# Kernel optimization log

Hardware: AMD Instinct MI355X
Metric: run time of the kernel (lower is better)

## Reference

```python
import jax, jax.numpy as jnp
import numpy as np

NUM_HEADS = 16
THETA = 10000.0


def _rope(x, pos):
    # x: (B, H, S, d_k), pos: (B, S) int
    d_k = x.shape[-1]
    freqs = 1.0 / (THETA ** (jnp.arange(0, d_k, 2, dtype=jnp.float32) / d_k))  # (d_k/2,)
    angles = pos[..., None].astype(jnp.float32) * freqs  # (B, S, d_k/2)
    cos = jnp.cos(angles)[:, None, :, :]  # (B, 1, S, d_k/2) broadcast over heads
    sin = jnp.sin(angles)[:, None, :, :]
    x1 = x[..., 0::2]
    x2 = x[..., 1::2]
    out1 = x1 * cos - x2 * sin
    out2 = x1 * sin + x2 * cos
    # interleave back: (..., d_k/2, 2) -> (..., d_k)
    return jnp.stack((out1, out2), axis=-1).reshape(x.shape)


def setup_inputs() -> dict:
    key = jax.random.key(0)
    ks = jax.random.split(key, 6)
    B, S, D = 4, 2048, 1024
    x = jax.random.normal(ks[0], (B, S, D), dtype=jnp.float32)
    token_positions = jnp.sort(jax.random.randint(ks[1], (B, S), 0, S), axis=-1).astype(jnp.int32)
    Wq = jax.random.normal(ks[2], (D, D), dtype=jnp.float32) * (D ** -0.5)
    Wk = jax.random.normal(ks[3], (D, D), dtype=jnp.float32) * (D ** -0.5)
    Wv = jax.random.normal(ks[4], (D, D), dtype=jnp.float32) * (D ** -0.5)
    Wo = jax.random.normal(ks[5], (D, D), dtype=jnp.float32) * (D ** -0.5)
    return {"x": x, "token_positions": token_positions, "Wq": Wq, "Wk": Wk, "Wv": Wv, "Wo": Wo}


def reference(x, token_positions, Wq, Wk, Wv, Wo):
    B, S, D = x.shape
    H = NUM_HEADS
    d_k = D // H
    # projections: y = x @ W.T  (Linear stores weight as (d_out, d_in))
    q = jnp.einsum('bsd,od->bso', x, Wq).reshape(B, S, H, d_k).transpose(0, 2, 1, 3)
    k = jnp.einsum('bsd,od->bso', x, Wk).reshape(B, S, H, d_k).transpose(0, 2, 1, 3)
    v = jnp.einsum('bsd,od->bso', x, Wv).reshape(B, S, H, d_k).transpose(0, 2, 1, 3)
    q = _rope(q, token_positions)
    k = _rope(k, token_positions)
    scores = jnp.einsum('bhqd,bhkd->bhqk', q, k) / jnp.sqrt(jnp.float32(d_k))
    causal = jnp.tril(jnp.ones((S, S), dtype=bool))
    scores = jnp.where(causal, scores, -jnp.inf)
    attn = jax.nn.softmax(scores, axis=-1)
    attn = jnp.nan_to_num(attn, nan=0.0)
    out = jnp.einsum('bhqk,bhkd->bhqd', attn, v)
    out = out.transpose(0, 2, 1, 3).reshape(B, S, D)
    return jnp.einsum('bso,do->bsd', out, Wo)
```

## Files before the change

### kernel.cpp

```cpp
#include <hip/hip_runtime.h>
#include <stdint.h>

#define SEQ 2048
#define NH  16
#define DK  64
#define DM  1024
#define C2SM 0.18033688011112042f

typedef __bf16 bf16x8 __attribute__((ext_vector_type(8)));
typedef float  f32x4  __attribute__((ext_vector_type(4)));
typedef float  f32x16 __attribute__((ext_vector_type(16)));
typedef int    iv2    __attribute__((ext_vector_type(2)));
typedef void __attribute__((address_space(3))) lds_void;
typedef const void __attribute__((address_space(1))) glb_void;

__device__ __forceinline__ unsigned short f2b(float f) {
  unsigned int u = __float_as_uint(f);
  u += 0x7fffu + ((u >> 16) & 1u);
  return (unsigned short)(u >> 16);
}
__device__ __forceinline__ float b2f(unsigned short h) {
  return __uint_as_float(((unsigned int)h) << 16);
}
__device__ __forceinline__ void gload_lds16(const void* g, void* lds) {
  __builtin_amdgcn_global_load_lds((glb_void*)(uintptr_t)g,
                                   (lds_void*)(unsigned int)(uintptr_t)lds,
                                   16, 0, 0);
}
__device__ __forceinline__ unsigned int cvtpk(float lo, float hi) {
  unsigned int r;
  asm("v_cvt_pk_bf16_f32 %0, %1, %2" : "=v"(r) : "v"(lo), "v"(hi));
  return r;
}
__device__ __forceinline__ iv2 pl32swap(int a, int b) {
  return __builtin_amdgcn_permlane32_swap(a, b, false, false);
}

__global__ __launch_bounds__(256) void k_cvt(const float* __restrict__ src,
                                             unsigned short* __restrict__ dst, int n4) {
  int i = blockIdx.x * 256 + threadIdx.x;
  if (i >= n4) return;
  float4 v = ((const float4*)src)[i];
  uint2 o;
  o.x = (unsigned int)f2b(v.x) | ((unsigned int)f2b(v.y) << 16);
  o.y = (unsigned int)f2b(v.z) | ((unsigned int)f2b(v.w) << 16);
  ((uint2*)dst)[i] = o;
}

__global__ __launch_bounds__(256) void k_cvtw(const float* __restrict__ w0,
                                              const float* __restrict__ w1,
                                              const float* __restrict__ w2,
                                              const float* __restrict__ w3,
                                              unsigned short* __restrict__ dst) {
  int i = blockIdx.x * 256 + threadIdx.x;
  const float* s = (i < 524288) ? ((i < 262144) ? w0 : w1)
                                : ((i < 786432) ? w2 : w3);
  float4 v = ((const float4*)s)[i & 262143];
  uint2 o;
  o.x = (unsigned int)f2b(v.x) | ((unsigned int)f2b(v.y) << 16);
  o.y = (unsigned int)f2b(v.z) | ((unsigned int)f2b(v.w) << 16);
  ((uint2*)dst)[i] = o;
}

__global__ __launch_bounds__(256) void k_tab(float2* __restrict__ tab) {
  int i = blockIdx.x * 256 + threadIdx.x;
  int p = i >> 5, f = i & 31;
  float freq = powf(10000.0f, -(float)(2 * f) / (float)DK);
  float ang = (float)p * freq;
  tab[i] = make_float2(cosf(ang), sinf(ang));
}

template <int MODE>
__global__ __launch_bounds__(256) void k_gemm(const unsigned short* __restrict__ A,
                                              const unsigned short* __restrict__ B,
                                              void* __restrict__ C, void* __restrict__ C2,
                                              const int* __restrict__ pos,
                                              const float2* __restrict__ tab,
                                              int M, int N, int K) {
  __shared__ __align__(16) unsigned short As[3][4096];
  __shared__ __align__(16) unsigned short Bs[3][4096];
  const int tid = threadIdx.x;
  const int wid = tid >> 6, lane = tid & 63;
  const int lr = lane & 15, lk = lane >> 4;
  const int wr = wid >> 1, wc = wid & 1;
  const int m0 = blockIdx.x * 128, n0 = blockIdx.y * 128;
  const int r0 = tid >> 2;
  const int csw = (((tid & 3) ^ ((r0 >> 1) & 3)) << 3);
  const int ss = ((lk ^ ((lr >> 1) & 3)) << 3);
  f32x4 acc[4][4] = {};

#define GSTAGE(bi, k0)                                                       \
  do {                                                                       \
    gload_lds16(A + (size_t)(m0 + r0) * K + (k0) + csw, &As[bi][wid * 512]); \
    gload_lds16(A + (size_t)(m0 + 64 + r0) * K + (k0) + csw,                 \
                &As[bi][2048 + wid * 512]);                                  \
    gload_lds16(B + (size_t)(n0 + r0) * K + (k0) + csw, &Bs[bi][wid * 512]); \
    gload_lds16(B + (size_t)(n0 + 64 + r0) * K + (k0) + csw,                 \
                &Bs[bi][2048 + wid * 512]);                                  \
  } while (0)

  const int nt = K >> 5;
  GSTAGE(0, 0);
  if (nt > 1) {
    GSTAGE(1, 32);
    asm volatile("s_waitcnt vmcnt(4)" ::: "memory");
  } else {
    asm volatile("s_waitcnt vmcnt(0)" ::: "memory");
  }
  __builtin_amdgcn_s_barrier();
  int c0 = 0, c1 = 1, c2 = 2;
  for (int t = 0; t < nt; ++t) {
    if (t + 2 < nt) GSTAGE(c2, (t + 2) * 32);
    bf16x8 af[4], bfv[4];
#pragma unroll
    for (int i = 0; i < 4; ++i)
      af[i] = *(const bf16x8*)&As[c0][(wr * 64 + i * 16 + lr) * 32 + ss];
#pragma unroll
    for (int j = 0; j < 4; ++j)
      bfv[j] = *(const bf16x8*)&Bs[c0][(wc * 64 + j * 16 + lr) * 32 + ss];
    __builtin_amdgcn_s_setprio(1);
#pragma unroll
    for (int i = 0; i < 4; ++i)
#pragma unroll
      for (int j = 0; j < 4; ++j)
        acc[i][j] = __builtin_amdgcn_mfma_f32_16x16x32_bf16(af[i], bfv[j], acc[i][j], 0, 0, 0);
    __builtin_amdgcn_s_setprio(0);
    if (t + 1 < nt) {
      if (t + 2 < nt)
        asm volatile("s_waitcnt vmcnt(4)" ::: "memory");
      else
        asm volatile("s_waitcnt vmcnt(0)" ::: "memory");
      __builtin_amdgcn_s_barrier();
    }
    int tmp = c0; c0 = c1; c1 = c2; c2 = tmp;
  }
#undef GSTAGE

  if (MODE == 1) {
#pragma unroll
    for (int i = 0; i < 4; ++i) {
      const int rbase = m0 + wr * 64 + i * 16 + lk * 4;
#pragma unroll
      for (int j = 0; j < 4; ++j) {
        const int col = n0 + wc * 64 + j * 16 + lr;
#pragma unroll
        for (int r = 0; r < 4; ++r)
          ((float*)C)[(size_t)(rbase + r) * N + col] = acc[i][j][r];
      }
    }
  } else {
    const int tt = n0 >> 10;
    if (tt == 2) {
#pragma unroll
      for (int i = 0; i < 4; ++i) {
        const int rbase = m0 + wr * 64 + i * 16 + lk * 4;
        const int bb = rbase >> 11;
        const int s0 = rbase & (SEQ - 1);
#pragma unroll
        for (int j = 0; j < 4; ++j) {
          const int col = n0 + wc * 64 + j * 16 + lr;
          const int h = (col >> 6) & 15, d = col & 63;
          uint2 pv;
          pv.x = cvtpk(acc[i][j][0], acc[i][j][1]);
          pv.y = cvtpk(acc[i][j][2], acc[i][j][3]);
          *(uint2*)&((unsigned short*)C2)[(((size_t)bb * NH + h) * DK + d) * SEQ + s0] = pv;
        }
      }
    } else {
#pragma unroll
      for (int i = 0; i < 4; ++i) {
        const int rbase = m0 + wr * 64 + i * 16 + lk * 4;
        const int bb = rbase >> 11;
        int prr[4];
#pragma unroll
        for (int r = 0; r < 4; ++r)
          prr[r] = pos[bb * SEQ + ((rbase + r) & (SEQ - 1))];
#pragma unroll
        for (int j = 0; j < 4; ++j) {
          const int col = n0 + wc * 64 + j * 16 + lr;
          const int h = (col >> 6) & 15, d = col & 63;
          const int f = d >> 1;
#pragma unroll
          for (int r = 0; r < 4; ++r) {
            float v = acc[i][j][r];
            float pv = __shfl_xor(v, 1);
            float2 cs = tab[(size_t)prr[r] * 32 + f];
            float o = (d & 1) ? __builtin_fmaf(pv, cs.y, v * cs.x)
                              : __builtin_fmaf(-pv, cs.y, v * cs.x);
            const int s = (rbase + r) & (SEQ - 1);
            ((unsigned short*)C)[(size_t)tt * 8388608 +
                                 ((((size_t)bb * NH + h) * SEQ) + s) * DK + d] = f2b(o);
          }
        }
      }
    }
  }
}

__global__ __launch_bounds__(128) void k_attn(const unsigned short* __restrict__ Q,
                                              const unsigned short* __restrict__ K,
                                              const unsigned short* __restrict__ VT,
                                              unsigned short* __restrict__ O) {
  __shared__ __align__(16) unsigned short Ks[2][64 * 64];
  __shared__ __align__(16) unsigned short Vs[2][64 * 64];
  const int tid = threadIdx.x, wid = tid >> 6, lane = tid & 63;
  const int l31 = lane & 31, hi = lane >> 5;
  const int n = blockIdx.x;
  const int bh = n & 63;
  const int qt = 31 - (n >> 6);
  const unsigned short* Qp = Q + (size_t)bh * SEQ * DK;
  const unsigned short* Kp = K + (size_t)bh * SEQ * DK;
  const unsigned short* Vp = VT + (size_t)bh * DK * SEQ;
  const int b = bh >> 4, h = bh & (NH - 1);

#define STAGE(bi, kb)                                                          \
  do {                                                                         \
    _Pragma("unroll") for (int i = 0; i < 4; ++i) {                            \
      const int c = i * 128 + tid;                                             \
      const int row = c >> 3, sl = ((c & 7) ^ (row & 7)) << 3;                 \
      gload_lds16(Kp + (size_t)((kb) + row) * DK + sl,                         \
                  &Ks[bi][(i * 128 + wid * 64) * 8]);                          \
      gload_lds16(Vp + (size_t)row * SEQ + (kb) + sl,                          \
                  &Vs[bi][(i * 128 + wid * 64) * 8]);                          \
    }                                                                          \
  } while (0)

  const int qw = qt * 64 + wid * 32;
  const int qrow = qw + l31;
  bf16x8 qf[4];
#pragma unroll
  for (int ks = 0; ks < 4; ++ks)
    qf[ks] = *(const bf16x8*)&Qp[(size_t)qrow * DK + ks * 16 + hi * 8];
  f32x16 oacc[2] = {};
  float m_ = -1e30f, l_ = 0.f;
  const int ntiles = qt + 1;
  STAGE(0, 0);
  for (int kt = 0; kt < ntiles; ++kt) {
    const int cur = kt & 1;
    const int kb = kt * 64;
    if (kt + 1 < ntiles) {
      STAGE(cur ^ 1, kb + 64);
      asm volatile("s_waitcnt vmcnt(8)" ::: "memory");
    } else {
      asm volatile("s_waitcnt vmcnt(0)" ::: "memory");
    }
    __builtin_amdgcn_s_barrier();
    {
      f32x16 sa[2];
      __builtin_amdgcn_s_setprio(1);
#pragma unroll
      for (int kg = 0; kg < 2; ++kg) {
        const int krow = kg * 32 + l31;
        f32x16 z = {};
#pragma unroll
        for (int ks = 0; ks < 4; ++ks) {
          bf16x8 kf = *(const bf16x8*)((const char*)&Ks[cur][0] + krow * 128 +
                                       (((2 * ks + hi) ^ (krow & 7)) << 4));
          z = __builtin_amdgcn_mfma_f32_32x32x16_bf16(kf, qf[ks], z, 0, 0, 0);
        }
        sa[kg] = z;
      }
      __builtin_amdgcn_s_setprio(0);
      if (kb + 64 > qw) {
        const int th0 = qrow - kb - 4 * hi;
#pragma unroll
        for (int kg = 0; kg < 2; ++kg) {
          const int th = th0 - kg * 32;
#pragma unroll
          for (int r = 0; r < 16; ++r) {
            const int cst = (r & 3) + 8 * (r >> 2);
            if (cst > th) sa[kg][r] = -1e30f;
          }
        }
      }
      float mx;
      {
        float a0 = fmaxf(fmaxf(sa[0][0], sa[0][1]), fmaxf(sa[0][2], sa[0][3]));
        float a1 = fmaxf(fmaxf(sa[0][4], sa[0][5]), fmaxf(sa[0][6], sa[0][7]));
        float a2 = fmaxf(fmaxf(sa[0][8], sa[0][9]), fmaxf(sa[0][10], sa[0][11]));
        float a3 = fmaxf(fmaxf(sa[0][12], sa[0][13]), fmaxf(sa[0][14], sa[0][15]));
        float a4 = fmaxf(fmaxf(sa[1][0], sa[1][1]), fmaxf(sa[1][2], sa[1][3]));
        float a5 = fmaxf(fmaxf(sa[1][4], sa[1][5]), fmaxf(sa[1][6], sa[1][7]));
        float a6 = fmaxf(fmaxf(sa[1][8], sa[1][9]), fmaxf(sa[1][10], sa[1][11]));
        float a7 = fmaxf(fmaxf(sa[1][12], sa[1][13]), fmaxf(sa[1][14], sa[1][15]));
        mx = fmaxf(fmaxf(fmaxf(a0, a1), fmaxf(a2, a3)),
                   fmaxf(fmaxf(a4, a5), fmaxf(a6, a7)));
        iv2 t = pl32swap(__float_as_int(mx), __float_as_int(mx));
        mx = fmaxf(__int_as_float(t.x), __int_as_float(t.y));
      }
      if (!__all(mx <= m_ + 16.f)) {
        const float mn = fmaxf(m_, mx);
        const float sc = __builtin_amdgcn_exp2f((m_ - mn) * C2SM);
        m_ = mn;
        l_ *= sc;
#pragma unroll
        for (int vg = 0; vg < 2; ++vg)
#pragma unroll
          for (int r = 0; r < 16; ++r) oacc[vg][r] *= sc;
      }
      const float mc = m_ * C2SM;
      float sum = 0.f;
#pragma unroll
      for (int kg = 0; kg < 2; ++kg)
#pragma unroll
        for (int r = 0; r < 16; ++r) {
          const float p = __builtin_amdgcn_exp2f(__builtin_fmaf(sa[kg][r], C2SM, -mc));
          sa[kg][r] = p;
          sum += p;
        }
      {
        iv2 t = pl32swap(__float_as_int(sum), __float_as_int(sum));
        l_ += __int_as_float(t.x) + __int_as_float(t.y);
      }
      __builtin_amdgcn_s_setprio(1);
#pragma unroll
      for (int kg = 0; kg < 2; ++kg)
#pragma unroll
        for (int ks2 = 0; ks2 < 2; ++ks2) {
          const int rb = ks2 * 8;
          unsigned wA = cvtpk(sa[kg][rb + 0], sa[kg][rb + 1]);
          unsigned wB = cvtpk(sa[kg][rb + 4], sa[kg][rb + 5]);
          unsigned wC = cvtpk(sa[kg][rb + 2], sa[kg][rb + 3]);
          unsigned wD = cvtpk(sa[kg][rb + 6], sa[kg][rb + 7]);
          iv2 r0 = pl32swap((int)wA, (int)wB);
          iv2 r1 = pl32swap((int)wC, (int)wD);
          union { uint4 u; bf16x8 v; } pu;
          pu.u = make_uint4((unsigned)r0.x, (unsigned)r1.x, (unsigned)r0.y, (unsigned)r1.y);
          const int ks = kg * 2 + ks2;
#pragma unroll
          for (int vg = 0; vg < 2; ++vg) {
            const int vrow = vg * 32 + l31;
            bf16x8 vf = *(const bf16x8*)((const char*)&Vs[cur][0] + vrow * 128 +
                                         (((2 * ks + hi) ^ (vrow & 7)) << 4));
            oacc[vg] = __builtin_amdgcn_mfma_f32_32x32x16_bf16(vf, pu.v, oacc[vg], 0, 0, 0);
          }
        }
      __builtin_amdgcn_s_setprio(0);
    }
    __builtin_amdgcn_s_barrier();
  }
  const float inv = 1.0f / l_;
  unsigned short* Orow = O + ((size_t)(b * SEQ + qrow)) * DM + h * DK;
#pragma unroll
  for (int vg = 0; vg < 2; ++vg)
#pragma unroll
    for (int j = 0; j < 4; ++j) {
      unsigned lo = cvtpk(oacc[vg][4 * j + 0] * inv, oacc[vg][4 * j + 1] * inv);
      unsigned hh = cvtpk(oacc[vg][4 * j + 2] * inv, oacc[vg][4 * j + 3] * inv);
      *(uint2*)&Orow[vg * 32 + 8 * j + 4 * hi] = make_uint2(lo, hh);
    }
#undef STAGE
}

extern "C" void kernel_launch(void* const* d_in, const int* in_sizes, int n_in,
                              void* d_out, int out_size, void* d_ws, size_t ws_size,
                              hipStream_t stream) {
  const float* x = (const float*)d_in[0];
  const int* tp = (const int*)d_in[1];
  const float* W[4] = {(const float*)d_in[2], (const float*)d_in[3],
                       (const float*)d_in[4], (const float*)d_in[5]};
  unsigned short* xb = (unsigned short*)d_ws;
  unsigned short* wb0 = xb + (size_t)8192 * 1024;
  unsigned short* wb3 = wb0 + (size_t)3 * 1024 * 1024;
  float2* tab = (float2*)(wb0 + (size_t)4 * 1024 * 1024);
  unsigned short* Qb = (unsigned short*)(tab + SEQ * 32);
  unsigned short* Kb = Qb + (size_t)8192 * 1024;
  unsigned short* VTb = Kb + (size_t)8192 * 1024;
  unsigned short* Ob = VTb + (size_t)8192 * 1024;

  k_cvt<<<8192, 256, 0, stream>>>(x, xb, 2097152);
  k_cvtw<<<4096, 256, 0, stream>>>(W[0], W[1], W[2], W[3], wb0);
  k_tab<<<256, 256, 0, stream>>>(tab);
  k_gemm<3><<<dim3(64, 24), 256, 0, stream>>>(xb, wb0, Qb, VTb, tp, tab, 8192, 3072, 1024);
  k_attn<<<2048, 128, 0, stream>>>(Qb, Kb, VTb, Ob);
  k_gemm<1><<<dim3(64, 8), 256, 0, stream>>>(Ob, wb3, d_out, nullptr, nullptr, nullptr,
                                             8192, 1024, 1024);
}
```

Measured before the change: 178.7 us.

## Fuse prep kernels into one launch and remap GEMM tiles per XCD for L2 reuse

Merges the x conversion, weight conversion and RoPE table kernels into a single k_prep launch, which removes two kernel launches and their gaps. Both GEMMs now use a 1D grid whose block index is remapped so that the blocks landing on each of the 8 XCDs (round-robin dispatch) share the same row block of A and sweep the N tiles. This is meant to raise L2 hit rate on each XCD's private L2. The remap assumes round-robin XCD dispatch and hardcodes the grid shapes.

```diff
diff --git a/kernel.cpp b/kernel.cpp
--- a/kernel.cpp
+++ b/kernel.cpp
@@ -36,38 +36,38 @@
   return __builtin_amdgcn_permlane32_swap(a, b, false, false);
 }
 
-__global__ __launch_bounds__(256) void k_cvt(const float* __restrict__ src,
-                                             unsigned short* __restrict__ dst, int n4) {
-  int i = blockIdx.x * 256 + threadIdx.x;
-  if (i >= n4) return;
-  float4 v = ((const float4*)src)[i];
-  uint2 o;
-  o.x = (unsigned int)f2b(v.x) | ((unsigned int)f2b(v.y) << 16);
-  o.y = (unsigned int)f2b(v.z) | ((unsigned int)f2b(v.w) << 16);
-  ((uint2*)dst)[i] = o;
-}
-
-__global__ __launch_bounds__(256) void k_cvtw(const float* __restrict__ w0,
+__global__ __launch_bounds__(256) void k_prep(const float* __restrict__ x,
+                                              const float* __restrict__ w0,
                                               const float* __restrict__ w1,
                                               const float* __restrict__ w2,
                                               const float* __restrict__ w3,
-                                              unsigned short* __restrict__ dst) {
-  int i = blockIdx.x * 256 + threadIdx.x;
-  const float* s = (i < 524288) ? ((i < 262144) ? w0 : w1)
-                                : ((i < 786432) ? w2 : w3);
-  float4 v = ((const float4*)s)[i & 262143];
-  uint2 o;
-  o.x = (unsigned int)f2b(v.x) | ((unsigned int)f2b(v.y) << 16);
-  o.y = (unsigned int)f2b(v.z) | ((unsigned int)f2b(v.w) << 16);
-  ((uint2*)dst)[i] = o;
-}
-
-__global__ __launch_bounds__(256) void k_tab(float2* __restrict__ tab) {
-  int i = blockIdx.x * 256 + threadIdx.x;
-  int p = i >> 5, f = i & 31;
-  float freq = powf(10000.0f, -(float)(2 * f) / (float)DK);
-  float ang = (float)p * freq;
-  tab[i] = make_float2(cosf(ang), sinf(ang));
+                                              unsigned short* __restrict__ xb,
+                                              unsigned short* __restrict__ wb,
+                                              float2* __restrict__ tab) {
+  const int bid = blockIdx.x, tid = threadIdx.x;
+  if (bid < 8192) {
+    int i = bid * 256 + tid;
+    float4 v = ((const float4*)x)[i];
+    uint2 o;
+    o.x = (unsigned int)f2b(v.x) | ((unsigned int)f2b(v.y) << 16);
+    o.y = (unsigned int)f2b(v.z) | ((unsigned int)f2b(v.w) << 16);
+    ((uint2*)xb)[i] = o;
+  } else if (bid < 12288) {
+    int i = (bid - 8192) * 256 + tid;
+    const float* s = (i < 524288) ? ((i < 262144) ? w0 : w1)
+                                  : ((i < 786432) ? w2 : w3);
+    float4 v = ((const float4*)s)[i & 262143];
+    uint2 o;
+    o.x = (unsigned int)f2b(v.x) | ((unsigned int)f2b(v.y) << 16);
+    o.y = (unsigned int)f2b(v.z) | ((unsigned int)f2b(v.w) << 16);
+    ((uint2*)wb)[i] = o;
+  } else {
+    int i = (bid - 12288) * 256 + tid;
+    int p = i >> 5, f = i & 31;
+    float freq = powf(10000.0f, -(float)(2 * f) / (float)DK);
+    float ang = (float)p * freq;
+    tab[i] = make_float2(cosf(ang), sinf(ang));
+  }
 }
 
 template <int MODE>
@@ -83,7 +83,11 @@
   const int wid = tid >> 6, lane = tid & 63;
   const int lr = lane & 15, lk = lane >> 4;
   const int wr = wid >> 1, wc = wid & 1;
-  const int m0 = blockIdx.x * 128, n0 = blockIdx.y * 128;
+  const int n_ = blockIdx.x;
+  const int xcd = n_ & 7, ii = n_ >> 3;
+  const int bx = (MODE == 3) ? (xcd * 8 + ii / 24) : (xcd * 8 + (ii >> 3));
+  const int by = (MODE == 3) ? (ii % 24) : (ii & 7);
+  const int m0 = bx * 128, n0 = by * 128;
   const int r0 = tid >> 2;
   const int csw = (((tid & 3) ^ ((r0 >> 1) & 3)) << 3);
   const int ss = ((lk ^ ((lr >> 1) & 3)) << 3);
@@ -368,11 +372,9 @@
   unsigned short* VTb = Kb + (size_t)8192 * 1024;
   unsigned short* Ob = VTb + (size_t)8192 * 1024;
 
-  k_cvt<<<8192, 256, 0, stream>>>(x, xb, 2097152);
-  k_cvtw<<<4096, 256, 0, stream>>>(W[0], W[1], W[2], W[3], wb0);
-  k_tab<<<256, 256, 0, stream>>>(tab);
-  k_gemm<3><<<dim3(64, 24), 256, 0, stream>>>(xb, wb0, Qb, VTb, tp, tab, 8192, 3072, 1024);
+  k_prep<<<12544, 256, 0, stream>>>(x, W[0], W[1], W[2], W[3], xb, wb0, tab);
+  k_gemm<3><<<1536, 256, 0, stream>>>(xb, wb0, Qb, VTb, tp, tab, 8192, 3072, 1024);
   k_attn<<<2048, 128, 0, stream>>>(Qb, Kb, VTb, Ob);
-  k_gemm<1><<<dim3(64, 8), 256, 0, stream>>>(Ob, wb3, d_out, nullptr, nullptr, nullptr,
-                                             8192, 1024, 1024);
-}
+  k_gemm<1><<<512, 256, 0, stream>>>(Ob, wb3, d_out, nullptr, nullptr, nullptr,
+                                     8192, 1024, 1024);
+}
```

After: 187.5 us. +4.9%, slower.
